# Performance work log

Hardware: AMD Instinct MI355X
Metric: run time of the kernel (lower is better)

Reference implementation:

```python
import jax, jax.numpy as jnp
import numpy as np

N_HEAD = 16
ROPE_BASE = 10000.0


def rope_cache(T, dim):
    half = dim // 2
    inv_freq = 1.0 / (ROPE_BASE ** (jnp.arange(half, dtype=jnp.float32) / half))
    freqs = jnp.arange(T, dtype=jnp.float32)[:, None] * inv_freq[None, :]  # [T, half]
    cos = jnp.repeat(jnp.cos(freqs), 2, axis=-1)  # [T, dim]
    sin = jnp.repeat(jnp.sin(freqs), 2, axis=-1)
    return cos, sin


def apply_rope(x, cos, sin):
    # x: [B, H, T, hd]; cos/sin: [T, hd] broadcast over B,H
    x1 = x[..., ::2]
    x2 = x[..., 1::2]
    x_rot = jnp.stack([-x2, x1], axis=-1).reshape(x.shape)
    return x * cos + x_rot * sin


def setup_inputs() -> dict:
    key = jax.random.key(0)
    k1, k2, k3, k4 = jax.random.split(key, 4)
    C = 1024
    x = jax.random.normal(k1, (2, 2048, C), jnp.float32)
    w_qkv = jax.random.normal(k2, (3 * C, C), jnp.float32) * 0.02
    w_out = jax.random.normal(k3, (C, C), jnp.float32) * 0.02
    b_out = jax.random.normal(k4, (C,), jnp.float32) * 0.02
    return {"x": x, "w_qkv": w_qkv, "w_out": w_out, "b_out": b_out}


def reference(x, w_qkv, w_out, b_out):
    B, T, C = x.shape
    H = N_HEAD
    hd = C // H
    qkv = x @ w_qkv.T                              # [B, T, 3C]
    qkv = qkv.reshape(B, T, 3, H, hd).transpose(2, 0, 3, 1, 4)  # [3, B, H, T, hd]
    q, k, v = qkv[0], qkv[1], qkv[2]
    cos, sin = rope_cache(T, hd)
    q = apply_rope(q, cos, sin)
    k = apply_rope(k, cos, sin)
    scale = hd ** (-0.5)
    scores = jnp.einsum('bhqd,bhkd->bhqk', q, k) * scale       # [B, H, T, T]
    causal = jnp.tril(jnp.ones((T, T), dtype=bool))
    scores = jnp.where(causal, scores, jnp.float32(-jnp.inf))
    att = jax.nn.softmax(scores, axis=-1)
    out = jnp.einsum('bhqk,bhkd->bhqd', att, v)                # [B, H, T, hd]
    out = out.transpose(0, 2, 1, 3).reshape(B, T, C)
    return out @ w_out.T + b_out
```

## Files before the change

### kernel.cpp

```cpp
#include <hip/hip_runtime.h>
#include <math.h>

namespace {

typedef __attribute__((ext_vector_type(8))) short s16x8;
typedef __attribute__((ext_vector_type(4))) float f32x4;
typedef unsigned int u32;
typedef unsigned short u16;

constexpr int B_ = 2;
constexpr int T_ = 2048;
constexpr int C_ = 1024;
constexpr int H_ = 16;
constexpr float L2E = 1.44269504088896340736f;

__device__ inline u16 f2bf(float x) {
    __bf16 h = (__bf16)x;
    return __builtin_bit_cast(u16, h);
}
__device__ inline u32 packbf2(float a, float b) {
    return (u32)f2bf(a) | ((u32)f2bf(b) << 16);
}
__device__ inline void gload_lds16(const void* g, void* lds) {
    __builtin_amdgcn_global_load_lds(
        (const __attribute__((address_space(1))) unsigned int*)g,
        (__attribute__((address_space(3))) unsigned int*)lds, 16, 0, 0);
}

#define VMW(n) asm volatile("s_waitcnt vmcnt(" #n ")" ::: "memory")
#define LGW0() asm volatile("s_waitcnt lgkmcnt(0)" ::: "memory")
#define BARRIER() do { __builtin_amdgcn_s_barrier(); asm volatile("" ::: "memory"); } while (0)
#define SB0() __builtin_amdgcn_sched_barrier(0)
#define PRIO1() __builtin_amdgcn_s_setprio(1)
#define PRIO0() __builtin_amdgcn_s_setprio(0)

__global__ __launch_bounds__(256) void tab_k(float2* __restrict__ cs) {
    int idx = blockIdx.x * 256 + threadIdx.x;
    int t = idx >> 5, i = idx & 31;
    float inv = 1.0f / powf(10000.0f, (float)i / 32.0f);
    float ang = (float)t * inv;
    cs[idx] = make_float2(cosf(ang), sinf(ang));
}

__global__ __launch_bounds__(256)
void cvt_k(const float4* __restrict__ x, const float4* __restrict__ wq,
           const float4* __restrict__ wo, uint2* __restrict__ xb,
           uint2* __restrict__ wqb, uint2* __restrict__ wob) {
    int i = blockIdx.x * 256 + threadIdx.x;
    const float4* s;
    uint2* d;
    int j;
    if (i < 1048576) { s = x; d = xb; j = i; }
    else if (i < 1048576 + 786432) { s = wq; d = wqb; j = i - 1048576; }
    else { s = wo; d = wob; j = i - (1048576 + 786432); }
    float4 v = s[j];
    d[j] = make_uint2(packbf2(v.x, v.y), packbf2(v.z, v.w));
}

__global__ __launch_bounds__(512, 2)
void qkv_mfma_k(const u16* __restrict__ xb, const u16* __restrict__ wqb,
                const float2* __restrict__ cs, u16* __restrict__ qb,
                u16* __restrict__ kb, u16* __restrict__ vt) {
    extern __shared__ char lds[];
    const int tid = threadIdx.x;
    const int w = tid >> 6, lane = tid & 63;
    const int c = lane & 15, g = lane >> 4;
    const int n0 = blockIdx.x * 256, m0 = blockIdx.y * 256;
    const int wr = w >> 2, wc = w & 3;

    f32x4 acc[8][4];
#pragma unroll
    for (int i = 0; i < 8; ++i)
#pragma unroll
        for (int j = 0; j < 4; ++j) acc[i][j] = (f32x4){0.f, 0.f, 0.f, 0.f};

    const u16* Ab = xb + (size_t)m0 * C_;
    const u16* Bb = wqb + (size_t)n0 * C_;
    const int srow = tid >> 3, sslot = tid & 7;

    auto stA = [&](int t, int hf) {
        char* base = lds + (((t & 1) * 2 + hf) << 14);
        const u16* src = Ab + (size_t)(hf * 128) * C_ + t * 64;
#pragma unroll
        for (int call = 0; call < 2; ++call) {
            int row = call * 64 + srow;
            int s = sslot ^ (row & 7);
            gload_lds16(src + (size_t)row * C_ + s * 8, base + call * 8192 + w * 1024);
        }
    };
    auto stB = [&](int t, int hf) {
        char* base = lds + 65536 + (((t & 1) * 2 + hf) << 14);
        const u16* src = Bb + (size_t)(hf * 128) * C_ + t * 64;
#pragma unroll
        for (int call = 0; call < 2; ++call) {
            int row = call * 64 + srow;
            int s = sslot ^ (row & 7);
            gload_lds16(src + (size_t)row * C_ + s * 8, base + call * 8192 + w * 1024);
        }
    };
    auto ldA = [&](int P, int mrep, int kh) -> s16x8 {
        const char* base = lds + ((P * 2 + wr) << 14);
        int row = mrep * 16 + c;
        return *(const s16x8*)(base + row * 128 + (((kh * 4 + g) ^ (row & 7)) * 16));
    };
    auto ldB = [&](int P, int nrep, int kh) -> s16x8 {
        int rowg = wc * 64 + nrep * 16 + c;
        int hf = rowg >> 7, row = rowg & 127;
        const char* base = lds + 65536 + ((P * 2 + hf) << 14);
        return *(const s16x8*)(base + row * 128 + (((kh * 4 + g) ^ (row & 7)) * 16));
    };

    s16x8 aA[4][2], bB0[2][2], bB1[2][2];

    stA(0, 0); stA(0, 1); stB(0, 0); stB(0, 1); stB(1, 0); stB(1, 1);
    VMW(4); BARRIER();

#pragma unroll 1
    for (int i = 0; i < 8; ++i) {
        const int tb_ = 2 * i + 1;
        const bool nl = (i < 7);
#pragma unroll
        for (int mm = 0; mm < 4; ++mm)
#pragma unroll
            for (int kh = 0; kh < 2; ++kh) aA[mm][kh] = ldA(0, mm, kh);
#pragma unroll
        for (int nn = 0; nn < 2; ++nn)
#pragma unroll
            for (int kh = 0; kh < 2; ++kh) bB0[nn][kh] = ldB(0, nn, kh);
        stA(tb_, 0);
        BARRIER(); LGW0(); SB0();
        PRIO1();
#pragma unroll
        for (int kh = 0; kh < 2; ++kh)
#pragma unroll
            for (int mm = 0; mm < 4; ++mm)
#pragma unroll
                for (int nn = 0; nn < 2; ++nn)
                    acc[mm][nn] = __builtin_amdgcn_mfma_f32_16x16x32_bf16(aA[mm][kh], bB0[nn][kh], acc[mm][nn], 0, 0, 0);
        PRIO0();
        BARRIER();
#pragma unroll
        for (int nn = 0; nn < 2; ++nn)
#pragma unroll
            for (int kh = 0; kh < 2; ++kh) bB1[nn][kh] = ldB(0, 2 + nn, kh);
        stA(tb_, 1);
        BARRIER(); LGW0(); SB0();
        PRIO1();
#pragma unroll
        for (int kh = 0; kh < 2; ++kh)
#pragma unroll
            for (int mm = 0; mm < 4; ++mm)
#pragma unroll
                for (int nn = 0; nn < 2; ++nn)
                    acc[mm][2 + nn] = __builtin_amdgcn_mfma_f32_16x16x32_bf16(aA[mm][kh], bB1[nn][kh], acc[mm][2 + nn], 0, 0, 0);
        PRIO0();
        BARRIER();
#pragma unroll
        for (int mm = 0; mm < 4; ++mm)
#pragma unroll
            for (int kh = 0; kh < 2; ++kh) aA[mm][kh] = ldA(0, 4 + mm, kh);
        if (nl) stB(2 * i + 2, 0);
        BARRIER(); LGW0(); SB0();
        PRIO1();
#pragma unroll
        for (int kh = 0; kh < 2; ++kh)
#pragma unroll
            for (int mm = 0; mm < 4; ++mm)
#pragma unroll
                for (int nn = 0; nn < 2; ++nn)
                    acc[4 + mm][nn] = __builtin_amdgcn_mfma_f32_16x16x32_bf16(aA[mm][kh], bB0[nn][kh], acc[4 + mm][nn], 0, 0, 0);
        PRIO0();
        BARRIER();
        if (nl) { stB(2 * i + 2, 1); VMW(4); } else { VMW(0); }
        BARRIER(); SB0();
        PRIO1();
#pragma unroll
        for (int kh = 0; kh < 2; ++kh)
#pragma unroll
            for (int mm = 0; mm < 4; ++mm)
#pragma unroll
                for (int nn = 0; nn < 2; ++nn)
                    acc[4 + mm][2 + nn] = __builtin_amdgcn_mfma_f32_16x16x32_bf16(aA[mm][kh], bB1[nn][kh], acc[4 + mm][2 + nn], 0, 0, 0);
        PRIO0();
        BARRIER();
#pragma unroll
        for (int mm = 0; mm < 4; ++mm)
#pragma unroll
            for (int kh = 0; kh < 2; ++kh) aA[mm][kh] = ldA(1, mm, kh);
#pragma unroll
        for (int nn = 0; nn < 2; ++nn)
#pragma unroll
            for (int kh = 0; kh < 2; ++kh) bB0[nn][kh] = ldB(1, nn, kh);
        if (nl) stA(2 * i + 2, 0);
        BARRIER(); LGW0(); SB0();
        PRIO1();
#pragma unroll
        for (int kh = 0; kh < 2; ++kh)
#pragma unroll
            for (int mm = 0; mm < 4; ++mm)
#pragma unroll
                for (int nn = 0; nn < 2; ++nn)
                    acc[mm][nn] = __builtin_amdgcn_mfma_f32_16x16x32_bf16(aA[mm][kh], bB0[nn][kh], acc[mm][nn], 0, 0, 0);
        PRIO0();
        BARRIER();
#pragma unroll
        for (int nn = 0; nn < 2; ++nn)
#pragma unroll
            for (int kh = 0; kh < 2; ++kh) bB1[nn][kh] = ldB(1, 2 + nn, kh);
        if (nl) stA(2 * i + 2, 1);
        BARRIER(); LGW0(); SB0();
        PRIO1();
#pragma unroll
        for (int kh = 0; kh < 2; ++kh)
#pragma unroll
            for (int mm = 0; mm < 4; ++mm)
#pragma unroll
                for (int nn = 0; nn < 2; ++nn)
                    acc[mm][2 + nn] = __builtin_amdgcn_mfma_f32_16x16x32_bf16(aA[mm][kh], bB1[nn][kh], acc[mm][2 + nn], 0, 0, 0);
        PRIO0();
        BARRIER();
#pragma unroll
        for (int mm = 0; mm < 4; ++mm)
#pragma unroll
            for (int kh = 0; kh < 2; ++kh) aA[mm][kh] = ldA(1, 4 + mm, kh);
        if (nl) stB(2 * i + 3, 0);
        BARRIER(); LGW0(); SB0();
        PRIO1();
#pragma unroll
        for (int kh = 0; kh < 2; ++kh)
#pragma unroll
            for (int mm = 0; mm < 4; ++mm)
#pragma unroll
                for (int nn = 0; nn < 2; ++nn)
                    acc[4 + mm][nn] = __builtin_amdgcn_mfma_f32_16x16x32_bf16(aA[mm][kh], bB0[nn][kh], acc[4 + mm][nn], 0, 0, 0);
        PRIO0();
        BARRIER();
        if (nl) { stB(2 * i + 3, 1); VMW(4); }
        BARRIER(); SB0();
        PRIO1();
#pragma unroll
        for (int kh = 0; kh < 2; ++kh)
#pragma unroll
            for (int mm = 0; mm < 4; ++mm)
#pragma unroll
                for (int nn = 0; nn < 2; ++nn)
                    acc[4 + mm][2 + nn] = __builtin_amdgcn_mfma_f32_16x16x32_bf16(aA[mm][kh], bB1[nn][kh], acc[4 + mm][2 + nn], 0, 0, 0);
        PRIO0();
        BARRIER();
    }

    const int sec = n0 >> 10;
    const int hD = ((n0 & 1023) >> 6) + wc;
    const int b = m0 >> 11;
    const int t0w = (m0 & 2047) + wr * 128;
    const int bh = b * H_ + hD;
    if (sec < 2) {
        u16* dst = (sec == 0) ? qb : kb;
        const float qs = (sec == 0) ? 0.125f : 1.0f;
#pragma unroll
        for (int nf = 0; nf < 4; ++nf) {
            int d = nf * 16 + c;
            int ibase = nf * 8 + (c >> 1);
#pragma unroll
            for (int mf = 0; mf < 8; ++mf) {
#pragma unroll
                for (int r = 0; r < 4; ++r) {
                    int t = t0w + mf * 16 + g * 4 + r;
                    float own = acc[mf][nf][r];
                    float partner = __shfl_xor(own, 1);
                    float2 csv = cs[t * 32 + ibase];
                    float rot = (d & 1) ? (own * csv.x + partner * csv.y)
                                        : (own * csv.x - partner * csv.y);
                    rot *= qs;
                    float rothi = __shfl_xor(rot, 1);
                    if (!(d & 1))
                        *(u32*)(dst + ((size_t)bh * T_ + t) * 64 + d) = packbf2(rot, rothi);
                }
            }
        }
    } else {
#pragma unroll
        for (int nf = 0; nf < 4; ++nf) {
            int d = nf * 16 + c;
#pragma unroll
            for (int mf = 0; mf < 8; ++mf) {
                int tb2 = t0w + mf * 16 + g * 4;
                u32 lo = packbf2(acc[mf][nf][0], acc[mf][nf][1]);
                u32 hi = packbf2(acc[mf][nf][2], acc[mf][nf][3]);
                *(uint2*)(vt + ((size_t)bh * 64 + d) * T_ + tb2) = make_uint2(lo, hi);
            }
        }
    }
}

__global__ __launch_bounds__(256)
void flash_mfma_k(const u16* __restrict__ qb, const u16* __restrict__ kb,
                  const u16* __restrict__ vt, u16* __restrict__ attb) {
    __shared__ char lds[32768];
    char* Qs = lds;
    char* Ks = lds + 8192;
    char* Vs = lds + 16384;
    char* Ps = lds + 24576;
    const int tid = threadIdx.x, w = tid >> 6, lane = tid & 63;
    const int c = lane & 15, g = lane >> 4;
    const int bh = blockIdx.x;
    const int qi = 31 - blockIdx.y;
    const int q0 = qi * 64, q0w = q0 + w * 16;
    const u16* Qg = qb + ((size_t)bh * T_ + q0) * 64;
    const u16* Kg = kb + (size_t)bh * T_ * 64;
    const u16* Vg = vt + (size_t)bh * 64 * T_;

#pragma unroll
    for (int call = 0; call < 2; ++call) {
        int row = call * 32 + (tid >> 3);
        int ds = (tid & 7) ^ (row & 7);
        gload_lds16(Qg + (size_t)row * 64 + ds * 8, Qs + call * 4096 + w * 1024);
    }
    __syncthreads();

    s16x8 bQ[2];
#pragma unroll
    for (int kc = 0; kc < 2; ++kc) {
        int row = w * 16 + c;
        bQ[kc] = *(const s16x8*)(Qs + row * 128 + (((kc * 4 + g) ^ (row & 7)) * 16));
    }

    float m_ = -INFINITY, l_ = 0.f;
    f32x4 accO[4];
#pragma unroll
    for (int j = 0; j < 4; ++j) accO[j] = (f32x4){0.f, 0.f, 0.f, 0.f};

    const int nt = qi + 1;
    for (int kt = 0; kt < nt; ++kt) {
        __syncthreads();
        {
            int row = tid >> 3, slot = tid & 7;
#pragma unroll
            for (int call = 0; call < 2; ++call) {
                int r = call * 32 + row;
                int ds = slot ^ (r & 7);
                gload_lds16(Kg + (size_t)(kt * 64 + r) * 64 + ds * 8, Ks + call * 4096 + w * 1024);
                gload_lds16(Vg + (size_t)r * T_ + kt * 64 + ds * 8, Vs + call * 4096 + w * 1024);
            }
        }
        __syncthreads();

        f32x4 S[4];
#pragma unroll
        for (int mf = 0; mf < 4; ++mf) S[mf] = (f32x4){0.f, 0.f, 0.f, 0.f};
        s16x8 aK[4][2];
#pragma unroll
        for (int mf = 0; mf < 4; ++mf)
#pragma unroll
            for (int kc = 0; kc < 2; ++kc) {
                int row = mf * 16 + c;
                aK[mf][kc] = *(const s16x8*)(Ks + row * 128 + (((kc * 4 + g) ^ (row & 7)) * 16));
            }
#pragma unroll
        for (int kc = 0; kc < 2; ++kc)
#pragma unroll
            for (int mf = 0; mf < 4; ++mf)
                S[mf] = __builtin_amdgcn_mfma_f32_16x16x32_bf16(aK[mf][kc], bQ[kc], S[mf], 0, 0, 0);

        if (kt == qi) {
#pragma unroll
            for (int mf = 0; mf < 4; ++mf)
#pragma unroll
                for (int r = 0; r < 4; ++r) {
                    int kvg = kt * 64 + mf * 16 + g * 4 + r;
                    if (kvg > q0w + c) S[mf][r] = -INFINITY;
                }
        }

        float mx = -INFINITY;
#pragma unroll
        for (int mf = 0; mf < 4; ++mf)
#pragma unroll
            for (int r = 0; r < 4; ++r) mx = fmaxf(mx, S[mf][r]);
        mx = fmaxf(mx, __shfl_xor(mx, 16));
        mx = fmaxf(mx, __shfl_xor(mx, 32));
        float alpha = 1.0f;
        if (!__all(mx - m_ <= 8.0f)) {
            float mnew = fmaxf(m_, mx);
            alpha = exp2f((m_ - mnew) * L2E);
            m_ = mnew;
#pragma unroll
            for (int r = 0; r < 4; ++r) {
                float ar = __shfl(alpha, g * 4 + r);
#pragma unroll
                for (int nd = 0; nd < 4; ++nd) accO[nd][r] *= ar;
            }
        }
        float sum = 0.f;
#pragma unroll
        for (int mf = 0; mf < 4; ++mf)
#pragma unroll
            for (int r = 0; r < 4; ++r) {
                float p = exp2f((S[mf][r] - m_) * L2E);
                S[mf][r] = p;
                sum += p;
            }
        sum += __shfl_xor(sum, 16);
        sum += __shfl_xor(sum, 32);
        l_ = l_ * alpha + sum;

#pragma unroll
        for (int mf = 0; mf < 4; ++mf)
#pragma unroll
            for (int p2 = 0; p2 < 2; ++p2) {
                u32 v = packbf2(S[mf][2 * p2], S[mf][2 * p2 + 1]);
                int off = (mf * 16 + g * 4 + p2 * 2) * 2;
                *(u32*)(Ps + w * 2048 + c * 128 + (off ^ ((c & 7) << 4))) = v;
            }
        __threadfence_block();

        s16x8 aP[2], bV[4][2];
#pragma unroll
        for (int kc = 0; kc < 2; ++kc)
            aP[kc] = *(const s16x8*)(Ps + w * 2048 + c * 128 + (((kc * 4 + g) ^ (c & 7)) * 16));
#pragma unroll
        for (int nd = 0; nd < 4; ++nd)
#pragma unroll
            for (int kc = 0; kc < 2; ++kc) {
                int row = nd * 16 + c;
                bV[nd][kc] = *(const s16x8*)(Vs + row * 128 + (((kc * 4 + g) ^ (row & 7)) * 16));
            }
#pragma unroll
        for (int kc = 0; kc < 2; ++kc)
#pragma unroll
            for (int nd = 0; nd < 4; ++nd)
                accO[nd] = __builtin_amdgcn_mfma_f32_16x16x32_bf16(aP[kc], bV[nd][kc], accO[nd], 0, 0, 0);
    }

    const int hh = bh & 15;
    const int bb = bh >> 4;
#pragma unroll
    for (int r = 0; r < 4; ++r) {
        float linv = 1.0f / __shfl(l_, g * 4 + r);
        int t = q0w + g * 4 + r;
        size_t rowb = ((size_t)bb * T_ + t) * C_ + hh * 64;
#pragma unroll
        for (int nd = 0; nd < 4; ++nd)
            attb[rowb + nd * 16 + c] = f2bf(accO[nd][r] * linv);
    }
}

__global__ __launch_bounds__(256)
void proj_mfma_k(const u16* __restrict__ attb, const u16* __restrict__ wob,
                 const float* __restrict__ bias, float* __restrict__ out) {
    __shared__ char lds[49152];
    char* const b0 = lds;
    char* const b1 = lds + 16384;
    char* const b2 = lds + 32768;
    const int tid = threadIdx.x;
    const int w = tid >> 6, lane = tid & 63;
    const int c = lane & 15, g = lane >> 4;
    const int n0 = blockIdx.x * 128, m0 = blockIdx.y * 128;
    const int wr = w >> 1, wc = w & 1;

    f32x4 acc[4][4];
#pragma unroll
    for (int i = 0; i < 4; ++i)
#pragma unroll
        for (int j = 0; j < 4; ++j) acc[i][j] = (f32x4){0.f, 0.f, 0.f, 0.f};

    const u16* Ab = attb + (size_t)m0 * C_;
    const u16* Bb = wob + (size_t)n0 * C_;
    const int srow = tid >> 2, sslot = tid & 3;

    auto stage = [&](int t, char* base) {
        int k0 = t * 32;
#pragma unroll
        for (int call = 0; call < 2; ++call) {
            int r = call * 64 + srow;
            int ds = sslot ^ ((r >> 1) & 3);
            gload_lds16(Ab + (size_t)r * C_ + k0 + ds * 8, base + call * 4096 + w * 1024);
            gload_lds16(Bb + (size_t)r * C_ + k0 + ds * 8, base + 8192 + call * 4096 + w * 1024);
        }
    };
    auto compute = [&](const char* base) {
        s16x8 aF[4], bF[4];
#pragma unroll
        for (int mf = 0; mf < 4; ++mf) {
            int row = wr * 64 + mf * 16 + c;
            aF[mf] = *(const s16x8*)(base + row * 64 + ((g ^ ((row >> 1) & 3)) * 16));
        }
#pragma unroll
        for (int nf = 0; nf < 4; ++nf) {
            int row = wc * 64 + nf * 16 + c;
            bF[nf] = *(const s16x8*)(base + 8192 + row * 64 + ((g ^ ((row >> 1) & 3)) * 16));
        }
#pragma unroll
        for (int mf = 0; mf < 4; ++mf)
#pragma unroll
            for (int nf = 0; nf < 4; ++nf)
                acc[mf][nf] = __builtin_amdgcn_mfma_f32_16x16x32_bf16(aF[mf], bF[nf], acc[mf][nf], 0, 0, 0);
    };

    stage(0, b0);
    stage(1, b1);
#pragma unroll 1
    for (int t = 0; t < 30; t += 3) {
        VMW(4); BARRIER(); stage(t + 2, b2); compute(b0); LGW0();
        VMW(4); BARRIER(); stage(t + 3, b0); compute(b1); LGW0();
        VMW(4); BARRIER(); stage(t + 4, b1); compute(b2); LGW0();
    }
    VMW(4); BARRIER(); compute(b0); LGW0();
    VMW(0); BARRIER(); compute(b1);

#pragma unroll
    for (int nf = 0; nf < 4; ++nf) {
        int n = n0 + wc * 64 + nf * 16 + c;
        float bv = bias[n];
#pragma unroll
        for (int mf = 0; mf < 4; ++mf)
#pragma unroll
            for (int r = 0; r < 4; ++r) {
                int mrow = m0 + wr * 64 + mf * 16 + g * 4 + r;
                out[(size_t)mrow * C_ + n] = acc[mf][nf][r] + bv;
            }
    }
}

}

extern "C" void kernel_launch(void* const* d_in, const int* in_sizes, int n_in,
                              void* d_out, int out_size, void* d_ws, size_t ws_size,
                              hipStream_t stream) {
    const float* x     = (const float*)d_in[0];
    const float* w_qkv = (const float*)d_in[1];
    const float* w_out = (const float*)d_in[2];
    const float* b_out = (const float*)d_in[3];
    float* out = (float*)d_out;

    char* ws = (char*)d_ws;
    float2* cs = (float2*)ws;
    u16* xb   = (u16*)(ws + 524288);
    u16* wqb  = (u16*)(ws + 524288 + 8388608);
    u16* wob  = (u16*)(ws + 524288 + 8388608 + 6291456);
    u16* qb   = (u16*)(ws + 17301504);
    u16* kb   = (u16*)(ws + 25690112);
    u16* vt   = (u16*)(ws + 34078720);
    u16* attb = (u16*)(ws + 42467328);

    (void)hipFuncSetAttribute((const void*)qkv_mfma_k,
                              hipFuncAttributeMaxDynamicSharedMemorySize, 131072);

    tab_k<<<256, 256, 0, stream>>>(cs);
    cvt_k<<<8192, 256, 0, stream>>>((const float4*)x, (const float4*)w_qkv,
                                    (const float4*)w_out, (uint2*)xb, (uint2*)wqb, (uint2*)wob);
    qkv_mfma_k<<<dim3(12, 16), 512, 131072, stream>>>(xb, wqb, cs, qb, kb, vt);
    flash_mfma_k<<<dim3(32, 32), 256, 0, stream>>>(qb, kb, vt, attb);
    proj_mfma_k<<<dim3(8, 32), 256, 0, stream>>>(attb, wob, b_out, out);
}
```

Measured before the change: 206.5 us.

## Load Q, K, V fragments directly from global memory in flash kernel

The flash attention kernel stops staging Q, K and V tiles through shared memory with block-wide barriers. Each wave now reads its MFMA operand fragments straight from global memory into registers, and shared memory is kept only for the P tile. This removes both __syncthreads per KV tile and the LDS round trip, and cuts LDS use, which may allow more blocks per CU. The cost is that all four waves in a block load the same K/V tile separately, relying on L1/L2 to serve the repeats, and the global reads are less coalesced.

After: 286.5 us. +38.7%, slower.

```diff
diff --git a/kernel.cpp b/kernel.cpp
--- a/kernel.cpp
+++ b/kernel.cpp
@@ -296,34 +296,20 @@
 __global__ __launch_bounds__(256)
 void flash_mfma_k(const u16* __restrict__ qb, const u16* __restrict__ kb,
                   const u16* __restrict__ vt, u16* __restrict__ attb) {
-    __shared__ char lds[32768];
-    char* Qs = lds;
-    char* Ks = lds + 8192;
-    char* Vs = lds + 16384;
-    char* Ps = lds + 24576;
+    __shared__ char Ps[8192];
     const int tid = threadIdx.x, w = tid >> 6, lane = tid & 63;
     const int c = lane & 15, g = lane >> 4;
     const int bh = blockIdx.x;
     const int qi = 31 - blockIdx.y;
-    const int q0 = qi * 64, q0w = q0 + w * 16;
-    const u16* Qg = qb + ((size_t)bh * T_ + q0) * 64;
+    const int q0w = qi * 64 + w * 16;
+    const u16* Qg = qb + ((size_t)bh * T_ + q0w) * 64;
     const u16* Kg = kb + (size_t)bh * T_ * 64;
     const u16* Vg = vt + (size_t)bh * 64 * T_;
 
-#pragma unroll
-    for (int call = 0; call < 2; ++call) {
-        int row = call * 32 + (tid >> 3);
-        int ds = (tid & 7) ^ (row & 7);
-        gload_lds16(Qg + (size_t)row * 64 + ds * 8, Qs + call * 4096 + w * 1024);
-    }
-    __syncthreads();
-
     s16x8 bQ[2];
 #pragma unroll
-    for (int kc = 0; kc < 2; ++kc) {
-        int row = w * 16 + c;
-        bQ[kc] = *(const s16x8*)(Qs + row * 128 + (((kc * 4 + g) ^ (row & 7)) * 16));
-    }
+    for (int kc = 0; kc < 2; ++kc)
+        bQ[kc] = *(const s16x8*)(Qg + (size_t)c * 64 + (kc * 4 + g) * 8);
 
     float m_ = -INFINITY, l_ = 0.f;
     f32x4 accO[4];
@@ -332,30 +318,21 @@
 
     const int nt = qi + 1;
     for (int kt = 0; kt < nt; ++kt) {
-        __syncthreads();
-        {
-            int row = tid >> 3, slot = tid & 7;
-#pragma unroll
-            for (int call = 0; call < 2; ++call) {
-                int r = call * 32 + row;
-                int ds = slot ^ (r & 7);
-                gload_lds16(Kg + (size_t)(kt * 64 + r) * 64 + ds * 8, Ks + call * 4096 + w * 1024);
-                gload_lds16(Vg + (size_t)r * T_ + kt * 64 + ds * 8, Vs + call * 4096 + w * 1024);
-            }
-        }
-        __syncthreads();
+        s16x8 aK[4][2], bV[4][2];
+#pragma unroll
+        for (int mf = 0; mf < 4; ++mf)
+#pragma unroll
+            for (int kc = 0; kc < 2; ++kc)
+                aK[mf][kc] = *(const s16x8*)(Kg + (size_t)(kt * 64 + mf * 16 + c) * 64 + (kc * 4 + g) * 8);
+#pragma unroll
+        for (int nd = 0; nd < 4; ++nd)
+#pragma unroll
+            for (int kc = 0; kc < 2; ++kc)
+                bV[nd][kc] = *(const s16x8*)(Vg + (size_t)(nd * 16 + c) * T_ + kt * 64 + (kc * 4 + g) * 8);
 
         f32x4 S[4];
 #pragma unroll
         for (int mf = 0; mf < 4; ++mf) S[mf] = (f32x4){0.f, 0.f, 0.f, 0.f};
-        s16x8 aK[4][2];
-#pragma unroll
-        for (int mf = 0; mf < 4; ++mf)
-#pragma unroll
-            for (int kc = 0; kc < 2; ++kc) {
-                int row = mf * 16 + c;
-                aK[mf][kc] = *(const s16x8*)(Ks + row * 128 + (((kc * 4 + g) ^ (row & 7)) * 16));
-            }
 #pragma unroll
         for (int kc = 0; kc < 2; ++kc)
 #pragma unroll
@@ -414,17 +391,10 @@
             }
         __threadfence_block();
 
-        s16x8 aP[2], bV[4][2];
+        s16x8 aP[2];
 #pragma unroll
         for (int kc = 0; kc < 2; ++kc)
             aP[kc] = *(const s16x8*)(Ps + w * 2048 + c * 128 + (((kc * 4 + g) ^ (c & 7)) * 16));
-#pragma unroll
-        for (int nd = 0; nd < 4; ++nd)
-#pragma unroll
-            for (int kc = 0; kc < 2; ++kc) {
-                int row = nd * 16 + c;
-                bV[nd][kc] = *(const s16x8*)(Vs + row * 128 + (((kc * 4 + g) ^ (row & 7)) * 16));
-            }
 #pragma unroll
         for (int kc = 0; kc < 2; ++kc)
 #pragma unroll
```
